# Optimization experiments

Hardware: AMD Instinct MI355X
Metric: run time of the kernel (lower is better)

Reference implementation:

```python
import jax, jax.numpy as jnp
import numpy as np

P, N, F, H, D_HID = 3, 4096, 1024, 8, 8
EMBED = H * D_HID  # 64
ATT, C = 128, 16


def setup_inputs() -> dict:
    key = jax.random.key(0)
    ks = jax.random.split(key, 12)
    return {
        "inputs": jax.random.normal(ks[0], (P, N, F), jnp.float32),
        # bias_mat plays the role of an additive adjacency mask; random floats are fine for math checking
        "bias_mat": jax.random.normal(ks[1], (P, N, N), jnp.float32),
        "W": jax.random.normal(ks[2], (P, H, F, D_HID), jnp.float32) * 0.05,
        "a1_w": jax.random.normal(ks[3], (P, H, D_HID), jnp.float32) * 0.1,
        "a1_b": jax.random.normal(ks[4], (P, H), jnp.float32) * 0.1,
        "a2_w": jax.random.normal(ks[5], (P, H, D_HID), jnp.float32) * 0.1,
        "a2_b": jax.random.normal(ks[6], (P, H), jnp.float32) * 0.1,
        "h_bias": jnp.zeros((P, H, D_HID), jnp.float32),
        "Ws": jax.random.normal(ks[7], (EMBED, ATT), jnp.float32) * 0.1,
        "bs": jax.random.normal(ks[8], (ATT,), jnp.float32) * 0.1,
        "u": jax.random.normal(ks[9], (ATT,), jnp.float32) * 0.1,
        "Wc": jax.random.normal(ks[10], (EMBED, C), jnp.float32) * 0.05,
        "bc": jnp.zeros((C,), jnp.float32),
    }


def reference(inputs, bias_mat, W, a1_w, a1_b, a2_w, a2_b, h_bias, Ws, bs, u, Wc, bc):
    # inputs: [P,N,F], bias_mat: [P,N,N]
    embeds = []
    for p in range(inputs.shape[0]):  # small fixed loop over meta-paths
        seq = inputs[p]                                            # [N,F]
        fts = jnp.einsum('nf,hfd->hnd', seq, W[p])                 # shared projection, all heads
        f1 = jnp.einsum('hnd,hd->hn', fts, a1_w[p]) + a1_b[p][:, None]
        f2 = jnp.einsum('hnd,hd->hn', fts, a2_w[p]) + a2_b[p][:, None]
        logits = f1[:, :, None] + f2[:, None, :]                   # [H,N,N] additive attention
        coefs = jax.nn.softmax(jax.nn.leaky_relu(logits) + bias_mat[p][None], axis=-1)
        vals = jnp.einsum('hnm,hmd->hnd', coefs, fts) + h_bias[p][:, None, :]
        h = jax.nn.elu(vals)                                       # activation per head
        embeds.append(jnp.transpose(h, (1, 0, 2)).reshape(h.shape[1], -1))  # concat heads -> [N,H*d]
    multi = jnp.stack(embeds, axis=1)                              # [N,P,EMBED]
    # semantic (meta-path) attention
    v = jnp.tanh(multi @ Ws + bs)                                  # [N,P,ATT]
    alphas = jax.nn.softmax(v @ u, axis=-1)                        # [N,P]
    final = jnp.sum(multi * alphas[:, :, None], axis=1)            # [N,EMBED]
    # single final classifier head (mean over 1 head == identity)
    logits_out = final @ Wc + bc                                   # [N,C]
    return logits_out, final, alphas
```

## Files before the change

kernel.cpp:

```cpp
#include <hip/hip_runtime.h>

#define LOG2E 1.44269504088896f

typedef _Float16 f16;
typedef _Float16 f16x8 __attribute__((ext_vector_type(8)));
typedef float f32x4 __attribute__((ext_vector_type(4)));

#define NP 3
#define NN 4096
#define FF 1024
#define HH 8
#define DD 8
#define HD 64

#define OFF_F1S   0
#define OFF_F2S   393216
#define OFF_F2MAX 589824
#define OFF_FTST  590080
#define OFF_MULTI 2162944
#define OFF_FP0   2162944
#define OFF_FP1   5308672
#define SLAB_BYTES 3145728

#define OUT_FINAL 65536
#define OUT_ALPHA 327680

__global__ __launch_bounds__(256) void kA1(const float* __restrict__ inp,
                                           const float* __restrict__ W,
                                           char* __restrict__ ws) {
    __shared__ float At[32 * 34];
    __shared__ float Bt[32 * 64];
    const int tid = threadIdx.x;
    const int p = blockIdx.y;
    const int n0 = blockIdx.x * 32;
    const int kb0 = blockIdx.z * 16;

    const int tr = tid >> 4, tc = tid & 15;
    const int r0 = tr * 2, c0 = tc * 4;
    const int sr = tid >> 3, sak = (tid & 7) * 4;
    const int bk = tid >> 3, bh = tid & 7;

    const float* aP = inp + ((size_t)p * NN + n0 + sr) * FF + sak;
    const float* bP = W + (((size_t)p * HH + bh) * FF + bk) * DD;
    float* bDst = &Bt[bk * 64 + bh * 8];
    float* slab = (float*)(ws + OFF_FP0 + (size_t)blockIdx.z * SLAB_BYTES);

    float4 pa, pb0, pb1;

#define KA_ISSUE(kb) do { \
        pa = *(const float4*)(aP + (kb) * 32); \
        const float* bp_ = bP + (size_t)(kb) * 32 * DD; \
        pb0 = *(const float4*)(bp_); \
        pb1 = *(const float4*)(bp_ + 4); \
    } while (0)

#define KA_COMMIT() do { \
        At[(sak + 0) * 34 + sr] = pa.x; \
        At[(sak + 1) * 34 + sr] = pa.y; \
        At[(sak + 2) * 34 + sr] = pa.z; \
        At[(sak + 3) * 34 + sr] = pa.w; \
        *(float4*)(bDst) = pb0; \
        *(float4*)(bDst + 4) = pb1; \
    } while (0)

    float acc[2][4] = {};

    KA_ISSUE(kb0);
    KA_COMMIT();
    KA_ISSUE(kb0 + 1);
    __syncthreads();

    #pragma unroll 1
    for (int kb = 0; kb < 16; ++kb) {
        #pragma unroll
        for (int k = 0; k < 32; ++k) {
            float2 a2 = *(const float2*)&At[k * 34 + r0];
            float4 bv = *(const float4*)&Bt[k * 64 + c0];
            float bb4[4] = {bv.x, bv.y, bv.z, bv.w};
            #pragma unroll
            for (int j = 0; j < 4; ++j) {
                acc[0][j] += a2.x * bb4[j];
                acc[1][j] += a2.y * bb4[j];
            }
        }
        __syncthreads();
        if (kb < 15) {
            KA_COMMIT();
            if (kb < 14) KA_ISSUE(kb0 + kb + 2);
            __syncthreads();
        }
    }
#undef KA_ISSUE
#undef KA_COMMIT

    #pragma unroll
    for (int i = 0; i < 2; ++i) {
        float4 o;
        o.x = acc[i][0]; o.y = acc[i][1]; o.z = acc[i][2]; o.w = acc[i][3];
        *(float4*)(slab + ((size_t)p * NN + n0 + r0 + i) * HD + c0) = o;
    }
}

__global__ __launch_bounds__(256) void kAe(const float* __restrict__ a1w,
                                           const float* __restrict__ a1b,
                                           const float* __restrict__ a2w,
                                           const float* __restrict__ a2b,
                                           char* __restrict__ ws) {
    __shared__ float ftile[64 * 68];
    const int tid = threadIdx.x;
    const int p = blockIdx.y;
    const int n0 = blockIdx.x * 64;

    const float* s0 = (const float*)(ws + OFF_FP0) + ((size_t)p * NN + n0) * HD;
    const float* s1 = (const float*)(ws + OFF_FP1) + ((size_t)p * NN + n0) * HD;

    {
        const int base = tid * 16;
        const int row = base >> 6, col = base & 63;
        #pragma unroll
        for (int q = 0; q < 4; ++q) {
            float4 u = *(const float4*)(s0 + base + q * 4);
            float4 v = *(const float4*)(s1 + base + q * 4);
            float4 o;
            o.x = u.x + v.x; o.y = u.y + v.y; o.z = u.z + v.z; o.w = u.w + v.w;
            *(float4*)&ftile[row * 68 + col + q * 4] = o;
        }
    }
    __syncthreads();

    float* f1s = (float*)(ws + OFF_F1S);
    f16* f2s = (f16*)(ws + OFF_F2S);
    #pragma unroll
    for (int rep = 0; rep < 2; ++rep) {
        int task = tid + rep * 256;
        int row = task >> 3, h = task & 7;
        const float* fb = &ftile[row * 68 + h * 8];
        float s1v = a1b[p * HH + h], s2v = a2b[p * HH + h];
        #pragma unroll
        for (int d = 0; d < 8; ++d) {
            float v = fb[d];
            s1v += v * a1w[((size_t)p * HH + h) * DD + d];
            s2v += v * a2w[((size_t)p * HH + h) * DD + d];
        }
        f1s[((size_t)p * HH + h) * NN + n0 + row] = s1v * LOG2E;
        f2s[((size_t)p * HH + h) * NN + n0 + row] = (f16)(s2v * LOG2E);
    }
    {
        f16* ftsT = (f16*)(ws + OFF_FTST);
        int cc2 = tid >> 2, rq = (tid & 3) * 16;
        union { f16 h[16]; uint4 u[2]; } pk;
        #pragma unroll
        for (int i = 0; i < 16; ++i) pk.h[i] = (f16)ftile[(rq + i) * 68 + cc2];
        uint4* dst = (uint4*)(ftsT + ((size_t)p * HD + cc2) * NN + n0 + rq);
        dst[0] = pk.u[0];
        dst[1] = pk.u[1];
    }
}

__global__ __launch_bounds__(64) void kA2(char* __restrict__ ws) {
    const f16* f2s = (const f16*)(ws + OFF_F2S);
    float* fmax = (float*)(ws + OFF_F2MAX);
    int b = blockIdx.x;
    int lane = threadIdx.x;
    float v = -1e30f;
    #pragma unroll
    for (int it = 0; it < 8; ++it) {
        union { uint4 u; f16 h[8]; } t;
        t.u = *(const uint4*)(f2s + (size_t)b * NN + ((size_t)it * 64 + lane) * 8);
        #pragma unroll
        for (int j = 0; j < 8; ++j) v = fmaxf(v, (float)t.h[j]);
    }
    #pragma unroll
    for (int off = 32; off >= 1; off >>= 1) v = fmaxf(v, __shfl_xor(v, off, 64));
    if (lane == 0) fmax[b] = v;
}

__global__ __launch_bounds__(256, 3) void kB(const float* __restrict__ bias,
                                             const float* __restrict__ h_bias,
                                             char* __restrict__ ws) {
    __shared__ __align__(16) char smem[42768];
    f16* ftsL = (f16*)smem;
    float* f2L = (float*)(smem + 34320);

    const int tid = threadIdx.x;
    const int lane = tid & 63, wv = tid >> 6;
    const int c = lane & 15, kg = lane >> 4;
    const int p = blockIdx.y;
    const int n0 = blockIdx.x * 16;
    const int n = n0 + c;

    const float* f1s = (const float*)(ws + OFF_F1S);
    const f16* f2s = (const f16*)(ws + OFF_F2S);
    const float* fmax = (const float*)(ws + OFF_F2MAX);
    const f16* ftsG = (const f16*)(ws + OFF_FTST);
    float* multi = (float*)(ws + OFF_MULTI);

    float A1[8], B1[8];
    #pragma unroll
    for (int h = 0; h < 8; ++h) {
        float f1v = f1s[((size_t)p * 8 + h) * NN + n];
        float fm = fmax[p * 8 + h];
        float x = f1v + fm;
        float lr = fmaxf(x, 0.01f * x);
        float ub = lr + 8.0f * LOG2E;
        A1[h] = f1v - ub;
        B1[h] = fmaf(0.01f, f1v, -ub);
    }

    for (int i = tid; i < 264; i += 256) ftsL[64 * 264 + i] = (f16)1.0f;

    const int sg = tid >> 3, se = tid & 7;
    const int srow = sg & 7, sq = sg >> 3;
    const int f2r = tid >> 5, f2c = (tid & 31) * 8;

    const f16* ftsP = ftsG + (size_t)p * HD * NN + sq * 64 + se * 8;
    const f16* f2P = f2s + (size_t)p * 8 * NN + (size_t)f2r * NN + f2c;
    f16* ldst = ftsL + srow * 264 + sq * 64 + se * 8;

    const int rowsel = (c < 8) ? c * 264 : 64 * 264;
    const int hstep = (c < 8) ? 8 * 264 : 0;

    const float* bb_base = bias + ((size_t)p * NN + n) * NN + wv * 64 + kg * 8;

    f32x4 acc[8] = {};

    uint4 r0, r1, r2, r3, r4, r5, r6, r7, rv;

#define ISSUE(ch) do { \
        const f16* gs_ = ftsP + (ch) * 256; \
        r0 = *(const uint4*)(gs_ + (size_t)(srow +  0) * NN); \
        r1 = *(const uint4*)(gs_ + (size_t)(srow +  8) * NN); \
        r2 = *(const uint4*)(gs_ + (size_t)(srow + 16) * NN); \
        r3 = *(const uint4*)(gs_ + (size_t)(srow + 24) * NN); \
        r4 = *(const uint4*)(gs_ + (size_t)(srow + 32) * NN); \
        r5 = *(const uint4*)(gs_ + (size_t)(srow + 40) * NN); \
        r6 = *(const uint4*)(gs_ + (size_t)(srow + 48) * NN); \
        r7 = *(const uint4*)(gs_ + (size_t)(srow + 56) * NN); \
        rv = *(const uint4*)(f2P + (ch) * 256); \
    } while (0)

#define COMMIT() do { \
        *(uint4*)(ldst + 0 * 8 * 264) = r0; \
        *(uint4*)(ldst + 1 * 8 * 264) = r1; \
        *(uint4*)(ldst + 2 * 8 * 264) = r2; \
        *(uint4*)(ldst + 3 * 8 * 264) = r3; \
        *(uint4*)(ldst + 4 * 8 * 264) = r4; \
        *(uint4*)(ldst + 5 * 8 * 264) = r5; \
        *(uint4*)(ldst + 6 * 8 * 264) = r6; \
        *(uint4*)(ldst + 7 * 8 * 264) = r7; \
        union { uint4 u; f16 h[8]; } t16_; \
        t16_.u = rv; \
        float4 lo_, hi_; \
        lo_.x = (float)t16_.h[0]; lo_.y = (float)t16_.h[1]; \
        lo_.z = (float)t16_.h[2]; lo_.w = (float)t16_.h[3]; \
        hi_.x = (float)t16_.h[4]; hi_.y = (float)t16_.h[5]; \
        hi_.z = (float)t16_.h[6]; hi_.w = (float)t16_.h[7]; \
        *(float4*)(f2L + f2r * 264 + f2c) = lo_; \
        *(float4*)(f2L + f2r * 264 + f2c + 4) = hi_; \
    } while (0)

    ISSUE(0);
    COMMIT();
    ISSUE(1);
    float4 uA0 = *(const float4*)(bb_base);
    float4 uA1 = *(const float4*)(bb_base + 4);
    float4 uB0 = *(const float4*)(bb_base + 32);
    float4 uB1 = *(const float4*)(bb_base + 36);
    __syncthreads();

    #pragma unroll 1
    for (int ch = 0; ch < 16; ++ch) {
        const int chn = (ch + 1 < 16) ? ch + 1 : 15;
        const float* bpn = bb_base + chn * 256;
        float4 nA0 = *(const float4*)(bpn);
        float4 nA1 = *(const float4*)(bpn + 4);
        float4 nB0 = *(const float4*)(bpn + 32);
        float4 nB1 = *(const float4*)(bpn + 36);

        #pragma unroll
        for (int s = 0; s < 2; ++s) {
            const int mloc = wv * 64 + s * 32 + kg * 8;
            float4 bv0 = s ? uB0 : uA0;
            float4 bv1 = s ? uB1 : uA1;
            float bbl[8] = {bv0.x * LOG2E, bv0.y * LOG2E, bv0.z * LOG2E, bv0.w * LOG2E,
                            bv1.x * LOG2E, bv1.y * LOG2E, bv1.z * LOG2E, bv1.w * LOG2E};
            #pragma unroll
            for (int h = 0; h < 8; ++h) {
                const float* f2p = f2L + h * 264 + mloc;
                float4 f2a = *(const float4*)f2p;
                float4 f2b = *(const float4*)(f2p + 4);
                float f2arr[8] = {f2a.x, f2a.y, f2a.z, f2a.w, f2b.x, f2b.y, f2b.z, f2b.w};
                f16x8 bf = *(const f16x8*)(ftsL + rowsel + h * hstep + mloc);
                union { f16x8 v; f16 e[8]; } af;
                #pragma unroll
                for (int j = 0; j < 8; ++j) {
                    float t1 = f2arr[j] + A1[h];
                    float t2 = fmaf(0.01f, f2arr[j], B1[h]);
                    af.e[j] = (f16)__builtin_amdgcn_exp2f(fmaxf(t1, t2) + bbl[j]);
                }
                acc[h] = __builtin_amdgcn_mfma_f32_16x16x32_f16(af.v, bf, acc[h], 0, 0, 0);
            }
        }
        __syncthreads();
        if (ch < 15) {
            COMMIT();
            if (ch < 14) ISSUE(ch + 2);
            __syncthreads();
        }
        uA0 = nA0; uA1 = nA1; uB0 = nB0; uB1 = nB1;
    }
#undef ISSUE
#undef COMMIT

    float* red = (float*)smem;
    #pragma unroll
    for (int h = 0; h < 8; ++h) {
        if (c <= 8) {
            #pragma unroll
            for (int r = 0; r < 4; ++r)
                red[((wv * 8 + h) * 16 + kg * 4 + r) * 9 + c] = acc[h][r];
        }
    }
    __syncthreads();
    #pragma unroll
    for (int rep = 0; rep < 4; ++rep) {
        int idx = tid + rep * 256;
        int R = idx >> 6, hd = idx & 63;
        int h = hd >> 3, d = hd & 7;
        float v = 0.f, l = 0.f;
        #pragma unroll
        for (int w = 0; w < 4; ++w) {
            v += red[((w * 8 + h) * 16 + R) * 9 + d];
            l += red[((w * 8 + h) * 16 + R) * 9 + 8];
        }
        float o = v / l + h_bias[(p * 8 + h) * 8 + d];
        o = o > 0.f ? o : (__builtin_amdgcn_exp2f(o * LOG2E) - 1.0f);
        multi[((size_t)(n0 + R) * NP + p) * HD + hd] = o;
    }
}

__global__ __launch_bounds__(256) void kC(const float* __restrict__ Ws,
                                          const float* __restrict__ bsv,
                                          const float* __restrict__ uv,
                                          const float* __restrict__ Wc,
                                          const float* __restrict__ bcv,
                                          char* __restrict__ ws,
                                          float* __restrict__ out) {
    __shared__ float WsL[64 * 128];
    __shared__ float mult[16 * 3 * 64];
    __shared__ float WcL[64 * 16];
    __shared__ float uL[128], bsL[128], bcL[16];
    __shared__ float vred[16 * 3 * 16];
    __shared__ float alphaL[16 * 3];
    __shared__ float fin[16 * 64];
    const int tid = threadIdx.x;
    const int n0 = blockIdx.x * 16;
    const float* multi = (const float*)(ws + OFF_MULTI);

    for (int i = tid; i < 64 * 128; i += 256) WsL[i] = Ws[i];
    for (int i = tid; i < 3072; i += 256) mult[i] = multi[(size_t)n0 * 192 + i];
    for (int i = tid; i < 1024; i += 256) WcL[i] = Wc[i];
    if (tid < 128) { uL[tid] = uv[tid]; bsL[tid] = bsv[tid]; }
    if (tid < 16) bcL[tid] = bcv[tid];
    __syncthreads();

    const int nl = tid >> 4, j = tid & 15;
    for (int p = 0; p < 3; ++p) {
        float va[8] = {};
        for (int e = 0; e < 64; ++e) {
            float me = mult[(nl * 3 + p) * 64 + e];
            #pragma unroll
            for (int i = 0; i < 8; ++i) va[i] += me * WsL[e * 128 + j + 16 * i];
        }
        float part = 0.f;
        #pragma unroll
        for (int i = 0; i < 8; ++i) part += tanhf(va[i] + bsL[j + 16 * i]) * uL[j + 16 * i];
        vred[(nl * 3 + p) * 16 + j] = part;
    }
    __syncthreads();
    if (tid < 16) {
        float sc[3];
        for (int p = 0; p < 3; ++p) {
            float s = 0.f;
            for (int jj = 0; jj < 16; ++jj) s += vred[(tid * 3 + p) * 16 + jj];
            sc[p] = s;
        }
        float mx = fmaxf(sc[0], fmaxf(sc[1], sc[2]));
        float e0 = __builtin_amdgcn_exp2f((sc[0] - mx) * LOG2E);
        float e1 = __builtin_amdgcn_exp2f((sc[1] - mx) * LOG2E);
        float e2 = __builtin_amdgcn_exp2f((sc[2] - mx) * LOG2E);
        float inv = 1.f / (e0 + e1 + e2);
        float a0 = e0 * inv, a1 = e1 * inv, a2 = e2 * inv;
        alphaL[tid * 3 + 0] = a0; alphaL[tid * 3 + 1] = a1; alphaL[tid * 3 + 2] = a2;
        out[OUT_ALPHA + (size_t)(n0 + tid) * 3 + 0] = a0;
        out[OUT_ALPHA + (size_t)(n0 + tid) * 3 + 1] = a1;
        out[OUT_ALPHA + (size_t)(n0 + tid) * 3 + 2] = a2;
    }
    __syncthreads();
    for (int idx = tid; idx < 1024; idx += 256) {
        int nn2 = idx >> 6, e = idx & 63;
        float f = 0.f;
        for (int p = 0; p < 3; ++p) f += mult[(nn2 * 3 + p) * 64 + e] * alphaL[nn2 * 3 + p];
        fin[nn2 * 64 + e] = f;
        out[OUT_FINAL + (size_t)(n0 + nn2) * 64 + e] = f;
    }
    __syncthreads();
    {
        int nn2 = tid >> 4, cc2 = tid & 15;
        float lg = bcL[cc2];
        for (int e = 0; e < 64; ++e) lg += fin[nn2 * 64 + e] * WcL[e * 16 + cc2];
        out[(size_t)(n0 + nn2) * 16 + cc2] = lg;
    }
}

extern "C" void kernel_launch(void* const* d_in, const int* in_sizes, int n_in,
                              void* d_out, int out_size, void* d_ws, size_t ws_size,
                              hipStream_t stream) {
    (void)in_sizes; (void)n_in; (void)out_size; (void)ws_size;
    const float* inp = (const float*)d_in[0];
    const float* bias = (const float*)d_in[1];
    const float* W = (const float*)d_in[2];
    const float* a1w = (const float*)d_in[3];
    const float* a1b = (const float*)d_in[4];
    const float* a2w = (const float*)d_in[5];
    const float* a2b = (const float*)d_in[6];
    const float* hb = (const float*)d_in[7];
    const float* Wsv = (const float*)d_in[8];
    const float* bsv = (const float*)d_in[9];
    const float* uv = (const float*)d_in[10];
    const float* Wcv = (const float*)d_in[11];
    const float* bcv = (const float*)d_in[12];
    char* ws = (char*)d_ws;
    float* out = (float*)d_out;

    hipLaunchKernelGGL(kA1, dim3(128, 3, 2), dim3(256), 0, stream, inp, W, ws);
    hipLaunchKernelGGL(kAe, dim3(64, 3), dim3(256), 0, stream, a1w, a1b, a2w, a2b, ws);
    hipLaunchKernelGGL(kA2, dim3(24), dim3(64), 0, stream, ws);
    hipLaunchKernelGGL(kB, dim3(256, 3), dim3(256), 0, stream, bias, hb, ws);
    hipLaunchKernelGGL(kC, dim3(256), dim3(256), 0, stream, Wsv, bsv, uv, Wcv, bcv, ws, out);
}
```

Measured before the change: 399.2 us.

## Double-buffer attention kernel LDS with single sync, retile projection GEMM

The attention kernel now streams keys in 128-wide chunks through two LDS buffers. This cuts the per-chunk barriers from two to one, and the all-ones operand comes from registers instead of LDS. Exponentials are packed to f16 in pairs with cvt_pkrtz, which rounds toward zero instead of to nearest. The projection GEMM uses 64-row tiles with a 4x4 register microtile and a 4-way K split, so the epilogue kernel now sums four partial slabs. The aim is less sync and LDS traffic, at the cost of more workspace slabs and a slightly different rounding mode.

```diff
diff --git a/kernel.cpp b/kernel.cpp
--- a/kernel.cpp
+++ b/kernel.cpp
@@ -3,6 +3,7 @@
 #define LOG2E 1.44269504088896f
 
 typedef _Float16 f16;
+typedef __fp16 fp16v2 __attribute__((ext_vector_type(2)));
 typedef _Float16 f16x8 __attribute__((ext_vector_type(8)));
 typedef float f32x4 __attribute__((ext_vector_type(4)));
 
@@ -19,7 +20,6 @@
 #define OFF_FTST  590080
 #define OFF_MULTI 2162944
 #define OFF_FP0   2162944
-#define OFF_FP1   5308672
 #define SLAB_BYTES 3145728
 
 #define OUT_FINAL 65536
@@ -28,65 +28,71 @@
 __global__ __launch_bounds__(256) void kA1(const float* __restrict__ inp,
                                            const float* __restrict__ W,
                                            char* __restrict__ ws) {
-    __shared__ float At[32 * 34];
+    __shared__ float At[32 * 68];
     __shared__ float Bt[32 * 64];
     const int tid = threadIdx.x;
     const int p = blockIdx.y;
-    const int n0 = blockIdx.x * 32;
-    const int kb0 = blockIdx.z * 16;
+    const int n0 = blockIdx.x * 64;
+    const int kb0 = blockIdx.z * 8;
 
     const int tr = tid >> 4, tc = tid & 15;
-    const int r0 = tr * 2, c0 = tc * 4;
-    const int sr = tid >> 3, sak = (tid & 7) * 4;
+    const int r0 = tr * 4, c0 = tc * 4;
+    const int sr = tid >> 2, sak = (tid & 3) * 8;
     const int bk = tid >> 3, bh = tid & 7;
 
-    const float* aP = inp + ((size_t)p * NN + n0 + sr) * FF + sak;
-    const float* bP = W + (((size_t)p * HH + bh) * FF + bk) * DD;
+    const float* aP = inp + ((size_t)p * NN + n0 + sr) * FF + kb0 * 32 + sak;
+    const float* bP = W + (((size_t)p * HH + bh) * FF + kb0 * 32 + bk) * DD;
     float* bDst = &Bt[bk * 64 + bh * 8];
     float* slab = (float*)(ws + OFF_FP0 + (size_t)blockIdx.z * SLAB_BYTES);
 
-    float4 pa, pb0, pb1;
+    float4 pa0, pa1, pb0, pb1;
 
 #define KA_ISSUE(kb) do { \
-        pa = *(const float4*)(aP + (kb) * 32); \
+        const float* ap_ = aP + (kb) * 32; \
+        pa0 = *(const float4*)(ap_); \
+        pa1 = *(const float4*)(ap_ + 4); \
         const float* bp_ = bP + (size_t)(kb) * 32 * DD; \
         pb0 = *(const float4*)(bp_); \
         pb1 = *(const float4*)(bp_ + 4); \
     } while (0)
 
 #define KA_COMMIT() do { \
-        At[(sak + 0) * 34 + sr] = pa.x; \
-        At[(sak + 1) * 34 + sr] = pa.y; \
-        At[(sak + 2) * 34 + sr] = pa.z; \
-        At[(sak + 3) * 34 + sr] = pa.w; \
+        At[(sak + 0) * 68 + sr] = pa0.x; \
+        At[(sak + 1) * 68 + sr] = pa0.y; \
+        At[(sak + 2) * 68 + sr] = pa0.z; \
+        At[(sak + 3) * 68 + sr] = pa0.w; \
+        At[(sak + 4) * 68 + sr] = pa1.x; \
+        At[(sak + 5) * 68 + sr] = pa1.y; \
+        At[(sak + 6) * 68 + sr] = pa1.z; \
+        At[(sak + 7) * 68 + sr] = pa1.w; \
         *(float4*)(bDst) = pb0; \
         *(float4*)(bDst + 4) = pb1; \
     } while (0)
 
-    float acc[2][4] = {};
-
-    KA_ISSUE(kb0);
+    float acc[4][4] = {};
+
+    KA_ISSUE(0);
     KA_COMMIT();
-    KA_ISSUE(kb0 + 1);
+    KA_ISSUE(1);
     __syncthreads();
 
     #pragma unroll 1
-    for (int kb = 0; kb < 16; ++kb) {
+    for (int kb = 0; kb < 8; ++kb) {
         #pragma unroll
         for (int k = 0; k < 32; ++k) {
-            float2 a2 = *(const float2*)&At[k * 34 + r0];
+            float4 av = *(const float4*)&At[k * 68 + r0];
             float4 bv = *(const float4*)&Bt[k * 64 + c0];
+            float aa[4] = {av.x, av.y, av.z, av.w};
             float bb4[4] = {bv.x, bv.y, bv.z, bv.w};
             #pragma unroll
-            for (int j = 0; j < 4; ++j) {
-                acc[0][j] += a2.x * bb4[j];
-                acc[1][j] += a2.y * bb4[j];
-            }
+            for (int i = 0; i < 4; ++i)
+                #pragma unroll
+                for (int j = 0; j < 4; ++j) acc[i][j] += aa[i] * bb4[j];
         }
         __syncthreads();
-        if (kb < 15) {
+        if (kb < 7) {
             KA_COMMIT();
-            if (kb < 14) KA_ISSUE(kb0 + kb + 2);
+            if (kb < 6) KA_ISSUE(kb + 2);
             __syncthreads();
         }
     }
@@ -94,7 +100,7 @@
 #undef KA_COMMIT
 
     #pragma unroll
-    for (int i = 0; i < 2; ++i) {
+    for (int i = 0; i < 4; ++i) {
         float4 o;
         o.x = acc[i][0]; o.y = acc[i][1]; o.z = acc[i][2]; o.w = acc[i][3];
         *(float4*)(slab + ((size_t)p * NN + n0 + r0 + i) * HD + c0) = o;
@@ -111,8 +117,11 @@
     const int p = blockIdx.y;
     const int n0 = blockIdx.x * 64;
 
-    const float* s0 = (const float*)(ws + OFF_FP0) + ((size_t)p * NN + n0) * HD;
-    const float* s1 = (const float*)(ws + OFF_FP1) + ((size_t)p * NN + n0) * HD;
+    const size_t boff = ((size_t)p * NN + n0) * HD;
+    const float* s0 = (const float*)(ws + OFF_FP0 + 0 * SLAB_BYTES) + boff;
+    const float* s1 = (const float*)(ws + OFF_FP0 + 1 * SLAB_BYTES) + boff;
+    const float* s2 = (const float*)(ws + OFF_FP0 + 2 * SLAB_BYTES) + boff;
+    const float* s3 = (const float*)(ws + OFF_FP0 + 3 * SLAB_BYTES) + boff;
 
     {
         const int base = tid * 16;
@@ -121,8 +130,13 @@
         for (int q = 0; q < 4; ++q) {
             float4 u = *(const float4*)(s0 + base + q * 4);
             float4 v = *(const float4*)(s1 + base + q * 4);
+            float4 x = *(const float4*)(s2 + base + q * 4);
+            float4 y = *(const float4*)(s3 + base + q * 4);
             float4 o;
-            o.x = u.x + v.x; o.y = u.y + v.y; o.z = u.z + v.z; o.w = u.w + v.w;
+            o.x = (u.x + v.x) + (x.x + y.x);
+            o.y = (u.y + v.y) + (x.y + y.y);
+            o.z = (u.z + v.z) + (x.z + y.z);
+            o.w = (u.w + v.w) + (x.w + y.w);
             *(float4*)&ftile[row * 68 + col + q * 4] = o;
         }
     }
@@ -178,9 +192,7 @@
 __global__ __launch_bounds__(256, 3) void kB(const float* __restrict__ bias,
                                              const float* __restrict__ h_bias,
                                              char* __restrict__ ws) {
-    __shared__ __align__(16) char smem[42768];
-    f16* ftsL = (f16*)smem;
-    float* f2L = (float*)(smem + 34320);
+    __shared__ __align__(16) char smem[43520];
 
     const int tid = threadIdx.x;
     const int lane = tid & 63, wv = tid >> 6;
@@ -207,107 +219,99 @@
         B1[h] = fmaf(0.01f, f1v, -ub);
     }
 
-    for (int i = tid; i < 264; i += 256) ftsL[64 * 264 + i] = (f16)1.0f;
-
-    const int sg = tid >> 3, se = tid & 7;
-    const int srow = sg & 7, sq = sg >> 3;
-    const int f2r = tid >> 5, f2c = (tid & 31) * 8;
-
-    const f16* ftsP = ftsG + (size_t)p * HD * NN + sq * 64 + se * 8;
+    union { f16x8 v; unsigned short u[8]; } onesu;
+    #pragma unroll
+    for (int i = 0; i < 8; ++i) onesu.u[i] = 0x3C00;
+    const bool isones = (c >= 8);
+
+    const int srow = tid >> 4;
+    const int se = tid & 15;
+    const int f2r = tid >> 5;
+    const int f2c = (tid & 31) * 4;
+
+    const f16* ftsP = ftsG + (size_t)p * HD * NN + (size_t)srow * NN + se * 8;
     const f16* f2P = f2s + (size_t)p * 8 * NN + (size_t)f2r * NN + f2c;
-    f16* ldst = ftsL + srow * 264 + sq * 64 + se * 8;
-
-    const int rowsel = (c < 8) ? c * 264 : 64 * 264;
-    const int hstep = (c < 8) ? 8 * 264 : 0;
-
-    const float* bb_base = bias + ((size_t)p * NN + n) * NN + wv * 64 + kg * 8;
+    const int ldo = srow * 136 + se * 8;
+
+    const int mloc = wv * 32 + kg * 8;
+    const int rowsel = (c & 7) * 136;
+
+    const float* bb_base = bias + ((size_t)p * NN + n) * NN + mloc;
 
     f32x4 acc[8] = {};
 
-    uint4 r0, r1, r2, r3, r4, r5, r6, r7, rv;
+    uint4 r0, r1, r2, r3;
+    uint2 rv;
 
 #define ISSUE(ch) do { \
-        const f16* gs_ = ftsP + (ch) * 256; \
-        r0 = *(const uint4*)(gs_ + (size_t)(srow +  0) * NN); \
-        r1 = *(const uint4*)(gs_ + (size_t)(srow +  8) * NN); \
-        r2 = *(const uint4*)(gs_ + (size_t)(srow + 16) * NN); \
-        r3 = *(const uint4*)(gs_ + (size_t)(srow + 24) * NN); \
-        r4 = *(const uint4*)(gs_ + (size_t)(srow + 32) * NN); \
-        r5 = *(const uint4*)(gs_ + (size_t)(srow + 40) * NN); \
-        r6 = *(const uint4*)(gs_ + (size_t)(srow + 48) * NN); \
-        r7 = *(const uint4*)(gs_ + (size_t)(srow + 56) * NN); \
-        rv = *(const uint4*)(f2P + (ch) * 256); \
+        const f16* gs_ = ftsP + (ch) * 128; \
+        r0 = *(const uint4*)(gs_); \
+        r1 = *(const uint4*)(gs_ + (size_t)16 * NN); \
+        r2 = *(const uint4*)(gs_ + (size_t)32 * NN); \
+        r3 = *(const uint4*)(gs_ + (size_t)48 * NN); \
+        rv = *(const uint2*)(f2P + (ch) * 128); \
     } while (0)
 
-#define COMMIT() do { \
-        *(uint4*)(ldst + 0 * 8 * 264) = r0; \
-        *(uint4*)(ldst + 1 * 8 * 264) = r1; \
-        *(uint4*)(ldst + 2 * 8 * 264) = r2; \
-        *(uint4*)(ldst + 3 * 8 * 264) = r3; \
-        *(uint4*)(ldst + 4 * 8 * 264) = r4; \
-        *(uint4*)(ldst + 5 * 8 * 264) = r5; \
-        *(uint4*)(ldst + 6 * 8 * 264) = r6; \
-        *(uint4*)(ldst + 7 * 8 * 264) = r7; \
-        union { uint4 u; f16 h[8]; } t16_; \
-        t16_.u = rv; \
-        float4 lo_, hi_; \
-        lo_.x = (float)t16_.h[0]; lo_.y = (float)t16_.h[1]; \
-        lo_.z = (float)t16_.h[2]; lo_.w = (float)t16_.h[3]; \
-        hi_.x = (float)t16_.h[4]; hi_.y = (float)t16_.h[5]; \
-        hi_.z = (float)t16_.h[6]; hi_.w = (float)t16_.h[7]; \
-        *(float4*)(f2L + f2r * 264 + f2c) = lo_; \
-        *(float4*)(f2L + f2r * 264 + f2c + 4) = hi_; \
+#define COMMIT(buf) do { \
+        f16* fb_ = (f16*)(smem + (buf) * 17408) + ldo; \
+        *(uint4*)(fb_) = r0; \
+        *(uint4*)(fb_ + 16 * 136) = r1; \
+        *(uint4*)(fb_ + 32 * 136) = r2; \
+        *(uint4*)(fb_ + 48 * 136) = r3; \
+        union { uint2 u; f16 h[4]; } t_; \
+        t_.u = rv; \
+        float4 fv_; \
+        fv_.x = (float)t_.h[0]; fv_.y = (float)t_.h[1]; \
+        fv_.z = (float)t_.h[2]; fv_.w = (float)t_.h[3]; \
+        *(float4*)((float*)(smem + 34816 + (buf) * 4352) + f2r * 136 + f2c) = fv_; \
     } while (0)
 
     ISSUE(0);
-    COMMIT();
+    COMMIT(0);
     ISSUE(1);
     float4 uA0 = *(const float4*)(bb_base);
     float4 uA1 = *(const float4*)(bb_base + 4);
-    float4 uB0 = *(const float4*)(bb_base + 32);
-    float4 uB1 = *(const float4*)(bb_base + 36);
+    float4 vA0 = *(const float4*)(bb_base + 128);
+    float4 vA1 = *(const float4*)(bb_base + 132);
     __syncthreads();
 
     #pragma unroll 1
-    for (int ch = 0; ch < 16; ++ch) {
-        const int chn = (ch + 1 < 16) ? ch + 1 : 15;
-        const float* bpn = bb_base + chn * 256;
-        float4 nA0 = *(const float4*)(bpn);
-        float4 nA1 = *(const float4*)(bpn + 4);
-        float4 nB0 = *(const float4*)(bpn + 32);
-        float4 nB1 = *(const float4*)(bpn + 36);
-
-        #pragma unroll
-        for (int s = 0; s < 2; ++s) {
-            const int mloc = wv * 64 + s * 32 + kg * 8;
-            float4 bv0 = s ? uB0 : uA0;
-            float4 bv1 = s ? uB1 : uA1;
-            float bbl[8] = {bv0.x * LOG2E, bv0.y * LOG2E, bv0.z * LOG2E, bv0.w * LOG2E,
-                            bv1.x * LOG2E, bv1.y * LOG2E, bv1.z * LOG2E, bv1.w * LOG2E};
+    for (int ch = 0; ch < 32; ++ch) {
+        const int cur = ch & 1;
+        if (ch < 31) COMMIT(cur ^ 1);
+        if (ch < 30) ISSUE(ch + 2);
+        const int chn = (ch + 2 < 32) ? ch + 2 : 31;
+        const float* bpn = bb_base + chn * 128;
+        float4 wA0 = *(const float4*)(bpn);
+        float4 wA1 = *(const float4*)(bpn + 4);
+
+        const f16* fts_ = (const f16*)(smem + cur * 17408);
+        const float* f2_ = (const float*)(smem + 34816 + cur * 4352);
+
+        float bbl[8] = {uA0.x * LOG2E, uA0.y * LOG2E, uA0.z * LOG2E, uA0.w * LOG2E,
+                        uA1.x * LOG2E, uA1.y * LOG2E, uA1.z * LOG2E, uA1.w * LOG2E};
+        #pragma unroll
+        for (int h = 0; h < 8; ++h) {
+            const float* f2p = f2_ + h * 136 + mloc;
+            float4 f2a = *(const float4*)f2p;
+            float4 f2b = *(const float4*)(f2p + 4);
+            float f2arr[8] = {f2a.x, f2a.y, f2a.z, f2a.w, f2b.x, f2b.y, f2b.z, f2b.w};
+            f16x8 bf = *(const f16x8*)(fts_ + rowsel + h * 8 * 136 + mloc);
+            if (isones) bf = onesu.v;
+            union { f16x8 v; fp16v2 p2[4]; } af;
             #pragma unroll
-            for (int h = 0; h < 8; ++h) {
-                const float* f2p = f2L + h * 264 + mloc;
-                float4 f2a = *(const float4*)f2p;
-                float4 f2b = *(const float4*)(f2p + 4);
-                float f2arr[8] = {f2a.x, f2a.y, f2a.z, f2a.w, f2b.x, f2b.y, f2b.z, f2b.w};
-                f16x8 bf = *(const f16x8*)(ftsL + rowsel + h * hstep + mloc);
-                union { f16x8 v; f16 e[8]; } af;
-                #pragma unroll
-                for (int j = 0; j < 8; ++j) {
-                    float t1 = f2arr[j] + A1[h];
-                    float t2 = fmaf(0.01f, f2arr[j], B1[h]);
-                    af.e[j] = (f16)__builtin_amdgcn_exp2f(fmaxf(t1, t2) + bbl[j]);
-                }
-                acc[h] = __builtin_amdgcn_mfma_f32_16x16x32_f16(af.v, bf, acc[h], 0, 0, 0);
+            for (int jj = 0; jj < 4; ++jj) {
+                float x0 = f2arr[2 * jj], x1 = f2arr[2 * jj + 1];
+                float e0 = __builtin_amdgcn_exp2f(
+                    fmaxf(x0 + A1[h], fmaf(0.01f, x0, B1[h])) + bbl[2 * jj]);
+                float e1 = __builtin_amdgcn_exp2f(
+                    fmaxf(x1 + A1[h], fmaf(0.01f, x1, B1[h])) + bbl[2 * jj + 1]);
+                af.p2[jj] = __builtin_amdgcn_cvt_pkrtz(e0, e1);
             }
+            acc[h] = __builtin_amdgcn_mfma_f32_16x16x32_f16(af.v, bf, acc[h], 0, 0, 0);
         }
         __syncthreads();
-        if (ch < 15) {
-            COMMIT();
-            if (ch < 14) ISSUE(ch + 2);
-            __syncthreads();
-        }
-        uA0 = nA0; uA1 = nA1; uB0 = nB0; uB1 = nB1;
+        uA0 = vA0; uA1 = vA1; vA0 = wA0; vA1 = wA1;
     }
 #undef ISSUE
 #undef COMMIT
@@ -433,7 +437,7 @@
     char* ws = (char*)d_ws;
     float* out = (float*)d_out;
 
-    hipLaunchKernelGGL(kA1, dim3(128, 3, 2), dim3(256), 0, stream, inp, W, ws);
+    hipLaunchKernelGGL(kA1, dim3(64, 3, 4), dim3(256), 0, stream, inp, W, ws);
     hipLaunchKernelGGL(kAe, dim3(64, 3), dim3(256), 0, stream, a1w, a1b, a2w, a2b, ws);
     hipLaunchKernelGGL(kA2, dim3(24), dim3(64), 0, stream, ws);
     hipLaunchKernelGGL(kB, dim3(256, 3), dim3(256), 0, stream, bias, hb, ws);
```

New measurement: 449.2 us. +12.5%, slower.
